# Performance work log

Measured on AMD Instinct MI355X. Metric: run time of the kernel, lower is better.

## Reference

```python
import jax, jax.numpy as jnp
import numpy as np
import math

EMBED = 1024
HEADS = 16
B, S = 2, 1024

def setup_inputs() -> dict:
    key = jax.random.key(0)
    ks = jax.random.split(key, 6)
    sc = 1.0 / math.sqrt(EMBED)
    return {
        "x": jax.random.normal(ks[0], (B, S, EMBED), dtype=jnp.float32),
        "Wq": jax.random.normal(ks[1], (EMBED, EMBED), dtype=jnp.float32) * sc,
        "Wk": jax.random.normal(ks[2], (EMBED, EMBED), dtype=jnp.float32) * sc,
        "Wv": jax.random.normal(ks[3], (EMBED, EMBED), dtype=jnp.float32) * sc,
        "Wo": jax.random.normal(ks[4], (EMBED, EMBED), dtype=jnp.float32) * sc,
        "bo": jax.random.normal(ks[5], (EMBED,), dtype=jnp.float32) * sc,
        "heads": HEADS,
    }

def reference(x, Wq, Wk, Wv, Wo, bo, heads):
    nB, nS, nE = x.shape
    nH = heads
    nG = nE // nH  # effective number of 'heads' in this (quirky) module

    def split(W):
        # (B,S,E) -> (B,S,G,H) -> (B,G,S,H); per-head dim is nH (as in source)
        return (x @ W).reshape(nB, nS, nG, nH).transpose(0, 2, 1, 3)

    q, k, v = split(Wq), split(Wk), split(Wv)
    # scale uses k.size(-1) == heads, matching the source
    att = jnp.einsum('bgsh,bgth->bgst', q, k) / math.sqrt(nH)
    causal = jnp.tril(jnp.ones((nS, nS), dtype=bool))  # True = keep
    att = jnp.where(causal, att, -jnp.inf)
    att = jax.nn.softmax(att, axis=-1)
    y = jnp.einsum('bgst,bgth->bgsh', att, v)
    y = y.transpose(0, 2, 1, 3).reshape(nB, nS, nE)
    return y @ Wo + bo
```

## Files before the change

### kernel.cpp

```cpp
#include <hip/hip_runtime.h>
#include <hip/hip_bf16.h>
#include <stdint.h>

typedef __attribute__((ext_vector_type(8))) short bf16x8;
typedef __attribute__((ext_vector_type(4))) short bf16x4;
typedef __attribute__((ext_vector_type(4))) float f32x4;

#define NB 2
#define SEQ 1024
#define EMB 1024
#define NH 16
#define NG 64

#if defined(__has_builtin)
#if __has_builtin(__builtin_amdgcn_mfma_f32_16x16x16bf16_1k)
#define QK_1K 1
#else
#define QK_1K 0
#endif
#if __has_builtin(__builtin_amdgcn_exp2f)
#define EXP2(x) __builtin_amdgcn_exp2f(x)
#else
#define EXP2(x) exp2f(x)
#endif
#if __has_builtin(__builtin_amdgcn_rcpf)
#define RCP(x) __builtin_amdgcn_rcpf(x)
#else
#define RCP(x) (1.0f / (x))
#endif
#else
#define QK_1K 0
#define EXP2(x) exp2f(x)
#define RCP(x) (1.0f / (x))
#endif

__device__ __forceinline__ unsigned short f2bf(float f){
  uint32_t u = __float_as_uint(f);
  uint32_t r = (u + 0x7fffu + ((u >> 16) & 1u)) >> 16;
  return (unsigned short)r;
}

__device__ __forceinline__ uint32_t pack_bf2(float lo, float hi){
  uint32_t a = (__float_as_uint(lo) + 0x8000u) >> 16;
  uint32_t b = (__float_as_uint(hi) + 0x8000u) & 0xffff0000u;
  return a | b;
}

__device__ __forceinline__ void gld_lds16(const void* g, void* l){
  __builtin_amdgcn_global_load_lds((__attribute__((address_space(1))) void*)(uintptr_t)(g),
                                   (__attribute__((address_space(3))) void*)(l),
                                   16, 0, 0);
}


__global__ __launch_bounds__(256) void prep_kernel(
    const float* __restrict__ x,
    const float* __restrict__ W0, const float* __restrict__ W1,
    const float* __restrict__ W2, const float* __restrict__ W3,
    unsigned short* __restrict__ xb,
    unsigned short* __restrict__ wtAll)
{
  const int bid = blockIdx.x;
  if (bid < 2048){
    int i = (bid * 256 + threadIdx.x) * 4;
    float4 f = *(const float4*)(x + i);
    ushort4 o;
    o.x = f2bf(f.x); o.y = f2bf(f.y); o.z = f2bf(f.z); o.w = f2bf(f.w);
    *(ushort4*)(xb + i) = o;
    return;
  }
  __shared__ float tile[32][33];
  const int b2 = bid - 2048;
  const int z = b2 & 3;
  const int rest = b2 >> 2;
  const float* W = (z == 0) ? W0 : (z == 1) ? W1 : (z == 2) ? W2 : W3;
  unsigned short* o = wtAll + (size_t)z * EMB * EMB;
  const int n0 = (rest & 31) * 32, k0 = (rest >> 5) * 32;
  const int tx = threadIdx.x & 31, ty = threadIdx.x >> 5;
#pragma unroll
  for (int i = 0; i < 4; i++)
    tile[ty + 8*i][tx] = W[(size_t)(k0 + ty + 8*i) * EMB + n0 + tx];
  __syncthreads();
#pragma unroll
  for (int i = 0; i < 4; i++)
    o[(size_t)(n0 + ty + 8*i) * EMB + k0 + tx] = f2bf(tile[tx][ty + 8*i]);
}


template<int J>
__device__ __forceinline__ void stage_tile(const unsigned short* __restrict__ src,
                                           unsigned short* __restrict__ dst,
                                           int row0, int k0, int t){
#pragma unroll
  for (int j = 0; j < J; ++j){
    const int c = t + 256 * j;
    const int row = c >> 3;
    const int col8 = (c & 7) ^ (row & 7);
    gld_lds16(src + (size_t)(row0 + row) * 1024 + k0 + col8 * 8, dst + c * 8);
  }
}


__global__ __launch_bounds__(256) void gemm_qkv_kernel(
    const unsigned short* __restrict__ A,
    const unsigned short* __restrict__ WtAll,
    unsigned short* __restrict__ qws,
    unsigned short* __restrict__ kws,
    unsigned short* __restrict__ vws)
{
  __shared__ unsigned short As[2][64][64];
  __shared__ unsigned short Bs[2][3][64][64];
  const unsigned short* B0 = WtAll;
  const unsigned short* B1 = WtAll + (size_t)EMB * EMB;
  const unsigned short* B2 = WtAll + (size_t)2 * EMB * EMB;
  const int m0 = blockIdx.x * 64, n0 = blockIdx.y * 64;
  const int t = threadIdx.x;
  const int l = t & 63, w = t >> 6;
  const int wr = w >> 1, wc = w & 1;
  const int lr = l & 15, lk = l >> 4;
  const int sw0 = (lk ^ (lr & 7)) * 8;
  const int sw1 = ((lk + 4) ^ (lr & 7)) * 8;

  f32x4 acc[3][2][2];
#pragma unroll
  for (int z = 0; z < 3; z++)
#pragma unroll
    for (int m = 0; m < 2; m++)
#pragma unroll
      for (int n = 0; n < 2; n++)
#pragma unroll
        for (int r = 0; r < 4; r++) acc[z][m][n][r] = 0.f;

  stage_tile<2>(A,  &As[0][0][0],    m0, 0, t);
  stage_tile<2>(B0, &Bs[0][0][0][0], n0, 0, t);
  stage_tile<2>(B1, &Bs[0][1][0][0], n0, 0, t);
  stage_tile<2>(B2, &Bs[0][2][0][0], n0, 0, t);
  __syncthreads();
  int cur = 0;
  for (int kt = 0; kt < 16; ++kt){
    if (kt < 15){
      const int k1 = (kt + 1) * 64;
      stage_tile<2>(A,  &As[cur^1][0][0],    m0, k1, t);
      stage_tile<2>(B0, &Bs[cur^1][0][0][0], n0, k1, t);
      stage_tile<2>(B1, &Bs[cur^1][1][0][0], n0, k1, t);
      stage_tile<2>(B2, &Bs[cur^1][2][0][0], n0, k1, t);
    }
#pragma unroll
    for (int half = 0; half < 2; ++half){
      const int sw = half ? sw1 : sw0;
      bf16x8 af[2];
#pragma unroll
      for (int m = 0; m < 2; m++)
        af[m] = *(const bf16x8*)(&As[cur][wr*32 + m*16 + lr][sw]);
#pragma unroll
      for (int z = 0; z < 3; z++){
        bf16x8 bfr[2];
#pragma unroll
        for (int n = 0; n < 2; n++)
          bfr[n] = *(const bf16x8*)(&Bs[cur][z][wc*32 + n*16 + lr][sw]);
#pragma unroll
        for (int m = 0; m < 2; m++)
#pragma unroll
          for (int n = 0; n < 2; n++)
            acc[z][m][n] = __builtin_amdgcn_mfma_f32_16x16x32_bf16(af[m], bfr[n], acc[z][m][n], 0, 0, 0);
      }
    }
    __syncthreads();
    cur ^= 1;
  }

  unsigned short (*vtile)[72] = (unsigned short (*)[72])(&As[0][0][0]);

#pragma unroll
  for (int m = 0; m < 2; m++){
    const int rowb = m0 + wr*32 + m*16 + lk*4;
#pragma unroll
    for (int n = 0; n < 2; n++){
      const int col = n0 + wc*32 + n*16 + lr;
      const int g = col >> 4, h = col & 15;
#pragma unroll
      for (int r = 0; r < 4; r++){
        const int rr = rowb + r;
        const int b = rr >> 10, s = rr & 1023;
        const int bg = b * NG + g;
        qws[((size_t)bg * 1024 + s) * 16 + h] = f2bf(acc[0][m][n][r] * 0.36067376022f);
        kws[((size_t)bg * 1024 + s) * 16 + h] = f2bf(acc[1][m][n][r]);
        vtile[wc*32 + n*16 + lr][wr*32 + m*16 + lk*4 + r] = f2bf(acc[2][m][n][r]);
      }
    }
  }
  __syncthreads();
  {
    const int cl = t >> 2, sc = t & 3;
    const int col = n0 + cl, g = col >> 4, h = col & 15;
    const int b = m0 >> 10;
    const int s0 = (m0 & 1023) + sc * 16;
    const int bg = b * NG + g;
    const uint4* p = (const uint4*)(&vtile[cl][sc * 16]);
    const uint4 v0 = p[0], v1 = p[1];
    uint4* dst = (uint4*)(vws + ((size_t)bg * 16 + h) * 1024 + s0);
    dst[0] = v0; dst[1] = v1;
  }
}


__global__ __launch_bounds__(256) void gemm_out_kernel(
    const unsigned short* __restrict__ A,
    const unsigned short* __restrict__ Bw,
    const float* __restrict__ bo,
    float* __restrict__ out)
{
  __shared__ unsigned short As[2][64][64];
  __shared__ unsigned short Bs[2][64][64];
  const int m0 = blockIdx.x * 64, n0 = blockIdx.y * 64;
  const int t = threadIdx.x;
  const int l = t & 63, w = t >> 6;
  const int wr = w >> 1, wc = w & 1;
  const int lr = l & 15, lk = l >> 4;
  const int sw0 = (lk ^ (lr & 7)) * 8;
  const int sw1 = ((lk + 4) ^ (lr & 7)) * 8;

  f32x4 acc[2][2];
#pragma unroll
  for (int m = 0; m < 2; m++)
#pragma unroll
    for (int n = 0; n < 2; n++)
#pragma unroll
      for (int r = 0; r < 4; r++) acc[m][n][r] = 0.f;

  stage_tile<2>(A, &As[0][0][0], m0, 0, t);
  stage_tile<2>(Bw, &Bs[0][0][0], n0, 0, t);
  __syncthreads();
  int cur = 0;
  for (int kt = 0; kt < 16; ++kt){
    if (kt < 15){
      stage_tile<2>(A, &As[cur ^ 1][0][0], m0, (kt + 1) * 64, t);
      stage_tile<2>(Bw, &Bs[cur ^ 1][0][0], n0, (kt + 1) * 64, t);
    }
#pragma unroll
    for (int half = 0; half < 2; ++half){
      const int sw = half ? sw1 : sw0;
      bf16x8 af[2], bfr[2];
#pragma unroll
      for (int m = 0; m < 2; m++) af[m]  = *(const bf16x8*)(&As[cur][wr*32 + m*16 + lr][sw]);
#pragma unroll
      for (int n = 0; n < 2; n++) bfr[n] = *(const bf16x8*)(&Bs[cur][wc*32 + n*16 + lr][sw]);
#pragma unroll
      for (int m = 0; m < 2; m++)
#pragma unroll
        for (int n = 0; n < 2; n++)
          acc[m][n] = __builtin_amdgcn_mfma_f32_16x16x32_bf16(af[m], bfr[n], acc[m][n], 0, 0, 0);
    }
    __syncthreads();
    cur ^= 1;
  }

#pragma unroll
  for (int m = 0; m < 2; m++){
    const int rowb = m0 + wr*32 + m*16 + lk*4;
#pragma unroll
    for (int n = 0; n < 2; n++){
      const int col = n0 + wc*32 + n*16 + lr;
      const float bb = bo[col];
#pragma unroll
      for (int r = 0; r < 4; r++)
        out[(size_t)(rowb + r) * 1024 + col] = acc[m][n][r] + bb;
    }
  }
}


#if QK_1K
struct KF { bf16x4 f[4]; };
#else
struct KF { bf16x8 f[4]; };
#endif

__device__ __forceinline__ void attn_tile(
#if QK_1K
    const bf16x4& aq,
#else
    const bf16x8& aq,
#endif
    const KF& kc, const bf16x8& bv0, const bf16x8& bv1,
    f32x4& yacc0, f32x4& yacc1, f32x4& sfr0, f32x4& sfr1,
    unsigned short (*pw)[72],
    int c0, int nt, int tt, int lr, int lk, const bf16x8& bone)
{
  const int t0 = tt << 6;
  f32x4 sacc[4];
#pragma unroll
  for (int ts = 0; ts < 4; ++ts){
    f32x4 zc;
#pragma unroll
    for (int r = 0; r < 4; r++) zc[r] = 0.f;
#if QK_1K
    sacc[ts] = __builtin_amdgcn_mfma_f32_16x16x16bf16_1k(kc.f[ts], aq, zc, 0, 0, 0);
#else
    sacc[ts] = __builtin_amdgcn_mfma_f32_16x16x32_bf16(kc.f[ts], aq, zc, 0, 0, 0);
#endif
  }

  if (tt == nt - 1){
    const int qrow = c0 + lr;
#pragma unroll
    for (int ts = 0; ts < 4; ++ts){
      const int key0 = t0 + ts*16 + lk*4;
#pragma unroll
      for (int r = 0; r < 4; ++r)
        if (key0 + r > qrow) sacc[ts][r] = -1e30f;
    }
  }

#pragma unroll
  for (int ts = 0; ts < 4; ++ts){
    const float e0 = EXP2(sacc[ts][0]);
    const float e1 = EXP2(sacc[ts][1]);
    const float e2 = EXP2(sacc[ts][2]);
    const float e3 = EXP2(sacc[ts][3]);
    uint2 u; u.x = pack_bf2(e0, e1); u.y = pack_bf2(e2, e3);
    *(uint2*)(&pw[lr][ts*16 + lk*4]) = u;
  }

  const bf16x8 ap0 = *(const bf16x8*)(&pw[lr][lk * 8]);
  const bf16x8 ap1 = *(const bf16x8*)(&pw[lr][32 + lk * 8]);

  sfr0  = __builtin_amdgcn_mfma_f32_16x16x32_bf16(ap0, bone,  sfr0, 0, 0, 0);
  sfr1  = __builtin_amdgcn_mfma_f32_16x16x32_bf16(ap1, bone,  sfr1, 0, 0, 0);
  yacc0 = __builtin_amdgcn_mfma_f32_16x16x32_bf16(ap0, bv0, yacc0, 0, 0, 0);
  yacc1 = __builtin_amdgcn_mfma_f32_16x16x32_bf16(ap1, bv1, yacc1, 0, 0, 0);
}

__global__ __launch_bounds__(256, 4) void attn_kernel(
    const unsigned short* __restrict__ q,
    const unsigned short* __restrict__ k,
    const unsigned short* __restrict__ vt,
    unsigned short* __restrict__ y)
{
  const int blk = blockIdx.x;
  const int bg = blk & 127;
  const int pg = blk >> 7;
  const int t = threadIdx.x, w = t >> 6, l = t & 63;
  const int lr = l & 15, lk = l >> 4;
  const int wvv = 31 - (pg * 4 + w);
  const int cA = 2 * wvv;
  const int c0A = cA * 16, c0B = c0A + 16;
  const int nt = (cA >> 2) + 1;

  __shared__ unsigned short p_lds[8][16][72];
  unsigned short (*pwA)[72] = p_lds[w * 2];
  unsigned short (*pwB)[72] = p_lds[w * 2 + 1];

  const unsigned short* qb = q + (size_t)bg * 1024 * 16;
  const unsigned short* kb = k + (size_t)bg * 1024 * 16;
  const unsigned short* vb = vt + (size_t)bg * 16 * 1024;
  const int b = bg >> 6, g = bg & 63;

  bf16x8 bone;
#pragma unroll
  for (int i = 0; i < 8; i++) bone[i] = (short)0x3F80;

#if QK_1K
  const bf16x4 aqA = *(const bf16x4*)(qb + (size_t)(c0A + lr) * 16 + lk * 4);
  const bf16x4 aqB = *(const bf16x4*)(qb + (size_t)(c0B + lr) * 16 + lk * 4);
#else
  bf16x8 aqA, aqB;
#pragma unroll
  for (int i = 0; i < 8; i++){ aqA[i] = 0; aqB[i] = 0; }
  if (lk < 2){
    aqA = *(const bf16x8*)(qb + (size_t)(c0A + lr) * 16 + lk * 8);
    aqB = *(const bf16x8*)(qb + (size_t)(c0B + lr) * 16 + lk * 8);
  }
#endif

  f32x4 yA0, yA1, sA0, sA1, yB0, yB1, sB0, sB1;
#pragma unroll
  for (int r = 0; r < 4; r++){
    yA0[r] = yA1[r] = sA0[r] = sA1[r] = 0.f;
    yB0[r] = yB1[r] = sB0[r] = sB1[r] = 0.f;
  }

  KF kc, kn;
#if !QK_1K
#pragma unroll
  for (int ts = 0; ts < 4; ++ts)
#pragma unroll
    for (int i = 0; i < 8; i++){ kc.f[ts][i] = 0; kn.f[ts][i] = 0; }
#endif
#pragma unroll
  for (int ts = 0; ts < 4; ++ts){
#if QK_1K
    kc.f[ts] = *(const bf16x4*)(kb + (size_t)(ts*16 + lr) * 16 + lk * 4);
#else
    if (lk < 2) kc.f[ts] = *(const bf16x8*)(kb + (size_t)(ts*16 + lr) * 16 + lk * 8);
#endif
  }

  for (int tt = 0; tt < nt; ++tt){
    const int t0 = tt << 6;

    if (tt + 1 < nt){
      const int t1 = t0 + 64;
#pragma unroll
      for (int ts = 0; ts < 4; ++ts){
#if QK_1K
        kn.f[ts] = *(const bf16x4*)(kb + (size_t)(t1 + ts*16 + lr) * 16 + lk * 4);
#else
        if (lk < 2) kn.f[ts] = *(const bf16x8*)(kb + (size_t)(t1 + ts*16 + lr) * 16 + lk * 8);
#endif
      }
    }
    const bf16x8 bv0 = *(const bf16x8*)(vb + (size_t)lr * 1024 + t0 + lk * 8);
    const bf16x8 bv1 = *(const bf16x8*)(vb + (size_t)lr * 1024 + t0 + 32 + lk * 8);

    attn_tile(aqA, kc, bv0, bv1, yA0, yA1, sA0, sA1, pwA, c0A, nt, tt, lr, lk, bone);
    attn_tile(aqB, kc, bv0, bv1, yB0, yB1, sB0, sB1, pwB, c0B, nt, tt, lr, lk, bone);

    kc = kn;
  }

#pragma unroll
  for (int r = 0; r < 4; ++r){
    const int sAi = c0A + lk*4 + r;
    const float vA = (yA0[r] + yA1[r]) * RCP(sA0[r] + sA1[r]);
    y[((size_t)b * 1024 + sAi) * 1024 + g * 16 + lr] = f2bf(vA);
    const int sBi = c0B + lk*4 + r;
    const float vB = (yB0[r] + yB1[r]) * RCP(sB0[r] + sB1[r]);
    y[((size_t)b * 1024 + sBi) * 1024 + g * 16 + lr] = f2bf(vB);
  }
}


extern "C" void kernel_launch(void* const* d_in, const int* in_sizes, int n_in,
                              void* d_out, int out_size, void* d_ws, size_t ws_size,
                              hipStream_t stream)
{
  const float* x  = (const float*)d_in[0];
  const float* Wq = (const float*)d_in[1];
  const float* Wk = (const float*)d_in[2];
  const float* Wv = (const float*)d_in[3];
  const float* Wo = (const float*)d_in[4];
  const float* bo = (const float*)d_in[5];
  float* out = (float*)d_out;
  char* ws = (char*)d_ws;

  unsigned short* xb  = (unsigned short*)(ws);
  unsigned short* wt  = (unsigned short*)(ws + (4u << 20));
  unsigned short* qws = (unsigned short*)(ws + (12u << 20));
  unsigned short* kws = (unsigned short*)(ws + (16u << 20));
  unsigned short* vws = (unsigned short*)(ws + (20u << 20));
  unsigned short* yws = (unsigned short*)(ws);

  prep_kernel<<<6144, 256, 0, stream>>>(x, Wq, Wk, Wv, Wo, xb, wt);
  gemm_qkv_kernel<<<dim3(32, 16), 256, 0, stream>>>(xb, wt, qws, kws, vws);
  attn_kernel<<<1024, 256, 0, stream>>>(qws, kws, vws, yws);
  gemm_out_kernel<<<dim3(32, 16), 256, 0, stream>>>(yws, wt + (size_t)3 * 1024 * 1024, bo, out);
}
```

Baseline: 67.41 us.

## Fuse all four stages into one cooperative persistent kernel with grid syncs

Replaces the four separate launches (convert/transpose, QKV GEMM, attention, output GEMM) with one cooperative kernel of 512 blocks that loops over virtual blocks and separates the stages with grid.sync(). This removes the launch gaps between kernels. To fit two blocks per CU in 32KB of shared memory, the QKV GEMM k-tile is halved to 32. The original multi-kernel path remains as a fallback if occupancy is too low or the cooperative launch fails. The tradeoff is grid-barrier cost plus fewer resident blocks, which may slow the attention and GEMM phases.

```diff
diff --git a/kernel.cpp b/kernel.cpp
--- a/kernel.cpp
+++ b/kernel.cpp
@@ -1,6 +1,9 @@
 #include <hip/hip_runtime.h>
 #include <hip/hip_bf16.h>
+#include <hip/hip_cooperative_groups.h>
 #include <stdint.h>
+
+namespace cg = cooperative_groups;
 
 typedef __attribute__((ext_vector_type(8))) short bf16x8;
 typedef __attribute__((ext_vector_type(4))) short bf16x4;
@@ -50,6 +53,393 @@
   __builtin_amdgcn_global_load_lds((__attribute__((address_space(1))) void*)(uintptr_t)(g),
                                    (__attribute__((address_space(3))) void*)(l),
                                    16, 0, 0);
+}
+
+
+template<int J>
+__device__ __forceinline__ void stage_tile(const unsigned short* __restrict__ src,
+                                           unsigned short* __restrict__ dst,
+                                           int row0, int k0, int t){
+#pragma unroll
+  for (int j = 0; j < J; ++j){
+    const int c = t + 256 * j;
+    const int row = c >> 3;
+    const int col8 = (c & 7) ^ (row & 7);
+    gld_lds16(src + (size_t)(row0 + row) * 1024 + k0 + col8 * 8, dst + c * 8);
+  }
+}
+
+__device__ __forceinline__ void stage_tile32(const unsigned short* __restrict__ src,
+                                             unsigned short* __restrict__ dst,
+                                             int row0, int k0, int t){
+  const int row = t >> 2;
+  const int col8 = (t & 3) ^ (row & 3);
+  gld_lds16(src + (size_t)(row0 + row) * 1024 + k0 + col8 * 8, dst + t * 8);
+}
+
+
+#if QK_1K
+struct KF { bf16x4 f[4]; };
+#else
+struct KF { bf16x8 f[4]; };
+#endif
+
+__device__ __forceinline__ void attn_tile(
+#if QK_1K
+    const bf16x4& aq,
+#else
+    const bf16x8& aq,
+#endif
+    const KF& kc, const bf16x8& bv0, const bf16x8& bv1,
+    f32x4& yacc0, f32x4& yacc1, f32x4& sfr0, f32x4& sfr1,
+    unsigned short (*pw)[72],
+    int c0, int nt, int tt, int lr, int lk, const bf16x8& bone)
+{
+  const int t0 = tt << 6;
+  f32x4 sacc[4];
+#pragma unroll
+  for (int ts = 0; ts < 4; ++ts){
+    f32x4 zc;
+#pragma unroll
+    for (int r = 0; r < 4; r++) zc[r] = 0.f;
+#if QK_1K
+    sacc[ts] = __builtin_amdgcn_mfma_f32_16x16x16bf16_1k(kc.f[ts], aq, zc, 0, 0, 0);
+#else
+    sacc[ts] = __builtin_amdgcn_mfma_f32_16x16x32_bf16(kc.f[ts], aq, zc, 0, 0, 0);
+#endif
+  }
+
+  if (tt == nt - 1){
+    const int qrow = c0 + lr;
+#pragma unroll
+    for (int ts = 0; ts < 4; ++ts){
+      const int key0 = t0 + ts*16 + lk*4;
+#pragma unroll
+      for (int r = 0; r < 4; ++r)
+        if (key0 + r > qrow) sacc[ts][r] = -1e30f;
+    }
+  }
+
+#pragma unroll
+  for (int ts = 0; ts < 4; ++ts){
+    const float e0 = EXP2(sacc[ts][0]);
+    const float e1 = EXP2(sacc[ts][1]);
+    const float e2 = EXP2(sacc[ts][2]);
+    const float e3 = EXP2(sacc[ts][3]);
+    uint2 u; u.x = pack_bf2(e0, e1); u.y = pack_bf2(e2, e3);
+    *(uint2*)(&pw[lr][ts*16 + lk*4]) = u;
+  }
+
+  const bf16x8 ap0 = *(const bf16x8*)(&pw[lr][lk * 8]);
+  const bf16x8 ap1 = *(const bf16x8*)(&pw[lr][32 + lk * 8]);
+
+  sfr0  = __builtin_amdgcn_mfma_f32_16x16x32_bf16(ap0, bone,  sfr0, 0, 0, 0);
+  sfr1  = __builtin_amdgcn_mfma_f32_16x16x32_bf16(ap1, bone,  sfr1, 0, 0, 0);
+  yacc0 = __builtin_amdgcn_mfma_f32_16x16x32_bf16(ap0, bv0, yacc0, 0, 0, 0);
+  yacc1 = __builtin_amdgcn_mfma_f32_16x16x32_bf16(ap1, bv1, yacc1, 0, 0, 0);
+}
+
+__device__ __forceinline__ void attn_pair(
+    const unsigned short* __restrict__ q,
+    const unsigned short* __restrict__ k,
+    const unsigned short* __restrict__ vt,
+    unsigned short* __restrict__ y,
+    int bg, int wvv, int lr, int lk,
+    unsigned short (*pwA)[72], unsigned short (*pwB)[72])
+{
+  const int cA = 2 * wvv;
+  const int c0A = cA * 16, c0B = c0A + 16;
+  const int nt = (cA >> 2) + 1;
+
+  const unsigned short* qb = q + (size_t)bg * 1024 * 16;
+  const unsigned short* kb = k + (size_t)bg * 1024 * 16;
+  const unsigned short* vb = vt + (size_t)bg * 16 * 1024;
+  const int b = bg >> 6, g = bg & 63;
+
+  bf16x8 bone;
+#pragma unroll
+  for (int i = 0; i < 8; i++) bone[i] = (short)0x3F80;
+
+#if QK_1K
+  const bf16x4 aqA = *(const bf16x4*)(qb + (size_t)(c0A + lr) * 16 + lk * 4);
+  const bf16x4 aqB = *(const bf16x4*)(qb + (size_t)(c0B + lr) * 16 + lk * 4);
+#else
+  bf16x8 aqA, aqB;
+#pragma unroll
+  for (int i = 0; i < 8; i++){ aqA[i] = 0; aqB[i] = 0; }
+  if (lk < 2){
+    aqA = *(const bf16x8*)(qb + (size_t)(c0A + lr) * 16 + lk * 8);
+    aqB = *(const bf16x8*)(qb + (size_t)(c0B + lr) * 16 + lk * 8);
+  }
+#endif
+
+  f32x4 yA0, yA1, sA0, sA1, yB0, yB1, sB0, sB1;
+#pragma unroll
+  for (int r = 0; r < 4; r++){
+    yA0[r] = yA1[r] = sA0[r] = sA1[r] = 0.f;
+    yB0[r] = yB1[r] = sB0[r] = sB1[r] = 0.f;
+  }
+
+  KF kc, kn;
+#if !QK_1K
+#pragma unroll
+  for (int ts = 0; ts < 4; ++ts)
+#pragma unroll
+    for (int i = 0; i < 8; i++){ kc.f[ts][i] = 0; kn.f[ts][i] = 0; }
+#endif
+#pragma unroll
+  for (int ts = 0; ts < 4; ++ts){
+#if QK_1K
+    kc.f[ts] = *(const bf16x4*)(kb + (size_t)(ts*16 + lr) * 16 + lk * 4);
+#else
+    if (lk < 2) kc.f[ts] = *(const bf16x8*)(kb + (size_t)(ts*16 + lr) * 16 + lk * 8);
+#endif
+  }
+
+  for (int tt = 0; tt < nt; ++tt){
+    const int t0 = tt << 6;
+    if (tt + 1 < nt){
+      const int t1 = t0 + 64;
+#pragma unroll
+      for (int ts = 0; ts < 4; ++ts){
+#if QK_1K
+        kn.f[ts] = *(const bf16x4*)(kb + (size_t)(t1 + ts*16 + lr) * 16 + lk * 4);
+#else
+        if (lk < 2) kn.f[ts] = *(const bf16x8*)(kb + (size_t)(t1 + ts*16 + lr) * 16 + lk * 8);
+#endif
+      }
+    }
+    const bf16x8 bv0 = *(const bf16x8*)(vb + (size_t)lr * 1024 + t0 + lk * 8);
+    const bf16x8 bv1 = *(const bf16x8*)(vb + (size_t)lr * 1024 + t0 + 32 + lk * 8);
+
+    attn_tile(aqA, kc, bv0, bv1, yA0, yA1, sA0, sA1, pwA, c0A, nt, tt, lr, lk, bone);
+    attn_tile(aqB, kc, bv0, bv1, yB0, yB1, sB0, sB1, pwB, c0B, nt, tt, lr, lk, bone);
+
+    kc = kn;
+  }
+
+#pragma unroll
+  for (int r = 0; r < 4; ++r){
+    const int sAi = c0A + lk*4 + r;
+    const float vA = (yA0[r] + yA1[r]) * RCP(sA0[r] + sA1[r]);
+    y[((size_t)b * 1024 + sAi) * 1024 + g * 16 + lr] = f2bf(vA);
+    const int sBi = c0B + lk*4 + r;
+    const float vB = (yB0[r] + yB1[r]) * RCP(sB0[r] + sB1[r]);
+    y[((size_t)b * 1024 + sBi) * 1024 + g * 16 + lr] = f2bf(vB);
+  }
+}
+
+
+__global__ __launch_bounds__(256, 2) void mega_kernel(
+    const float* __restrict__ x,
+    const float* __restrict__ W0, const float* __restrict__ W1,
+    const float* __restrict__ W2, const float* __restrict__ W3,
+    const float* __restrict__ bo, float* __restrict__ out,
+    unsigned short* __restrict__ xb,
+    unsigned short* __restrict__ wt,
+    unsigned short* __restrict__ qws,
+    unsigned short* __restrict__ kws,
+    unsigned short* __restrict__ vws)
+{
+  cg::grid_group grid = cg::this_grid();
+  __shared__ __align__(16) unsigned char smem[32768];
+
+  const int blk = blockIdx.x;
+  const int t = threadIdx.x;
+  const int l = t & 63, w = t >> 6;
+  const int lr = l & 15, lk = l >> 4;
+
+  for (int vb = blk; vb < 6144; vb += 512){
+    if (vb < 2048){
+      const int i = (vb * 256 + t) * 4;
+      float4 f = *(const float4*)(x + i);
+      ushort4 o;
+      o.x = f2bf(f.x); o.y = f2bf(f.y); o.z = f2bf(f.z); o.w = f2bf(f.w);
+      *(ushort4*)(xb + i) = o;
+    } else {
+      float (*tile)[33] = (float (*)[33])smem;
+      const int b2 = vb - 2048;
+      const int z = b2 & 3;
+      const int rest = b2 >> 2;
+      const float* W = (z == 0) ? W0 : (z == 1) ? W1 : (z == 2) ? W2 : W3;
+      unsigned short* o = wt + (size_t)z * EMB * EMB;
+      const int n0 = (rest & 31) * 32, k0 = (rest >> 5) * 32;
+      const int tx = t & 31, ty = t >> 5;
+      __syncthreads();
+#pragma unroll
+      for (int i = 0; i < 4; i++)
+        tile[ty + 8*i][tx] = W[(size_t)(k0 + ty + 8*i) * EMB + n0 + tx];
+      __syncthreads();
+#pragma unroll
+      for (int i = 0; i < 4; i++)
+        o[(size_t)(n0 + ty + 8*i) * EMB + k0 + tx] = f2bf(tile[tx][ty + 8*i]);
+    }
+  }
+  grid.sync();
+
+  {
+    unsigned short (*As)[64][32] = (unsigned short (*)[64][32])smem;
+    unsigned short (*Bs)[3][64][32] = (unsigned short (*)[3][64][32])(smem + 8192);
+    const unsigned short* A = xb;
+    const unsigned short* B0 = wt;
+    const unsigned short* B1 = wt + (size_t)EMB * EMB;
+    const unsigned short* B2 = wt + (size_t)2 * EMB * EMB;
+    const int m0 = (blk >> 4) * 64, n0 = (blk & 15) * 64;
+    const int wr = w >> 1, wc = w & 1;
+    const int sw = (lk ^ (lr & 3)) * 8;
+
+    f32x4 acc[3][2][2];
+#pragma unroll
+    for (int z = 0; z < 3; z++)
+#pragma unroll
+      for (int m = 0; m < 2; m++)
+#pragma unroll
+        for (int n = 0; n < 2; n++)
+#pragma unroll
+          for (int r = 0; r < 4; r++) acc[z][m][n][r] = 0.f;
+
+    stage_tile32(A,  &As[0][0][0],    m0, 0, t);
+    stage_tile32(B0, &Bs[0][0][0][0], n0, 0, t);
+    stage_tile32(B1, &Bs[0][1][0][0], n0, 0, t);
+    stage_tile32(B2, &Bs[0][2][0][0], n0, 0, t);
+    __syncthreads();
+    int cur = 0;
+    for (int kt = 0; kt < 32; ++kt){
+      if (kt < 31){
+        const int k1 = (kt + 1) * 32;
+        stage_tile32(A,  &As[cur^1][0][0],    m0, k1, t);
+        stage_tile32(B0, &Bs[cur^1][0][0][0], n0, k1, t);
+        stage_tile32(B1, &Bs[cur^1][1][0][0], n0, k1, t);
+        stage_tile32(B2, &Bs[cur^1][2][0][0], n0, k1, t);
+      }
+      bf16x8 af[2];
+#pragma unroll
+      for (int m = 0; m < 2; m++)
+        af[m] = *(const bf16x8*)(&As[cur][wr*32 + m*16 + lr][sw]);
+#pragma unroll
+      for (int z = 0; z < 3; z++){
+        bf16x8 bfr[2];
+#pragma unroll
+        for (int n = 0; n < 2; n++)
+          bfr[n] = *(const bf16x8*)(&Bs[cur][z][wc*32 + n*16 + lr][sw]);
+#pragma unroll
+        for (int m = 0; m < 2; m++)
+#pragma unroll
+          for (int n = 0; n < 2; n++)
+            acc[z][m][n] = __builtin_amdgcn_mfma_f32_16x16x32_bf16(af[m], bfr[n], acc[z][m][n], 0, 0, 0);
+      }
+      __syncthreads();
+      cur ^= 1;
+    }
+
+    unsigned short (*vtile)[72] = (unsigned short (*)[72])smem;
+#pragma unroll
+    for (int m = 0; m < 2; m++){
+      const int rowb = m0 + wr*32 + m*16 + lk*4;
+#pragma unroll
+      for (int n = 0; n < 2; n++){
+        const int col = n0 + wc*32 + n*16 + lr;
+        const int g = col >> 4, h = col & 15;
+#pragma unroll
+        for (int r = 0; r < 4; r++){
+          const int rr = rowb + r;
+          const int b = rr >> 10, s = rr & 1023;
+          const int bg = b * NG + g;
+          qws[((size_t)bg * 1024 + s) * 16 + h] = f2bf(acc[0][m][n][r] * 0.36067376022f);
+          kws[((size_t)bg * 1024 + s) * 16 + h] = f2bf(acc[1][m][n][r]);
+          vtile[wc*32 + n*16 + lr][wr*32 + m*16 + lk*4 + r] = f2bf(acc[2][m][n][r]);
+        }
+      }
+    }
+    __syncthreads();
+    {
+      const int cl = t >> 2, sc = t & 3;
+      const int col = n0 + cl, g = col >> 4, h = col & 15;
+      const int b = m0 >> 10;
+      const int s0 = (m0 & 1023) + sc * 16;
+      const int bg = b * NG + g;
+      const uint4* p = (const uint4*)(&vtile[cl][sc * 16]);
+      const uint4 v0 = p[0], v1 = p[1];
+      uint4* dst = (uint4*)(vws + ((size_t)bg * 16 + h) * 1024 + s0);
+      dst[0] = v0; dst[1] = v1;
+    }
+  }
+  grid.sync();
+
+  {
+    unsigned short (*pl)[16][72] = (unsigned short (*)[16][72])smem;
+    unsigned short (*pwA)[72] = pl[w * 2];
+    unsigned short (*pwB)[72] = pl[w * 2 + 1];
+    const int bg = blk & 127;
+    const int g0 = blk >> 7;
+#pragma unroll
+    for (int it = 0; it < 2; ++it){
+      const int pgeff = it ? (7 - g0) : g0;
+      const int wvv = 31 - (pgeff * 4 + w);
+      attn_pair(qws, kws, vws, xb , bg, wvv, lr, lk, pwA, pwB);
+    }
+  }
+  grid.sync();
+
+  {
+    unsigned short (*As)[64][64] = (unsigned short (*)[64][64])smem;
+    unsigned short (*Bs)[64][64] = (unsigned short (*)[64][64])(smem + 16384);
+    const unsigned short* A = xb;
+    const unsigned short* Bw = wt + (size_t)3 * EMB * EMB;
+    const int m0 = (blk >> 4) * 64, n0 = (blk & 15) * 64;
+    const int wr = w >> 1, wc = w & 1;
+    const int sw0 = (lk ^ (lr & 7)) * 8;
+    const int sw1 = ((lk + 4) ^ (lr & 7)) * 8;
+
+    f32x4 acc[2][2];
+#pragma unroll
+    for (int m = 0; m < 2; m++)
+#pragma unroll
+      for (int n = 0; n < 2; n++)
+#pragma unroll
+        for (int r = 0; r < 4; r++) acc[m][n][r] = 0.f;
+
+    __syncthreads();
+    stage_tile<2>(A,  &As[0][0][0], m0, 0, t);
+    stage_tile<2>(Bw, &Bs[0][0][0], n0, 0, t);
+    __syncthreads();
+    int cur = 0;
+    for (int kt = 0; kt < 16; ++kt){
+      if (kt < 15){
+        stage_tile<2>(A,  &As[cur ^ 1][0][0], m0, (kt + 1) * 64, t);
+        stage_tile<2>(Bw, &Bs[cur ^ 1][0][0], n0, (kt + 1) * 64, t);
+      }
+#pragma unroll
+      for (int half = 0; half < 2; ++half){
+        const int sw = half ? sw1 : sw0;
+        bf16x8 af[2], bfr[2];
+#pragma unroll
+        for (int m = 0; m < 2; m++) af[m]  = *(const bf16x8*)(&As[cur][wr*32 + m*16 + lr][sw]);
+#pragma unroll
+        for (int n = 0; n < 2; n++) bfr[n] = *(const bf16x8*)(&Bs[cur][wc*32 + n*16 + lr][sw]);
+#pragma unroll
+        for (int m = 0; m < 2; m++)
+#pragma unroll
+          for (int n = 0; n < 2; n++)
+            acc[m][n] = __builtin_amdgcn_mfma_f32_16x16x32_bf16(af[m], bfr[n], acc[m][n], 0, 0, 0);
+      }
+      __syncthreads();
+      cur ^= 1;
+    }
+
+#pragma unroll
+    for (int m = 0; m < 2; m++){
+      const int rowb = m0 + wr*32 + m*16 + lk*4;
+#pragma unroll
+      for (int n = 0; n < 2; n++){
+        const int col = n0 + wc*32 + n*16 + lr;
+        const float bb = bo[col];
+#pragma unroll
+        for (int r = 0; r < 4; r++)
+          out[(size_t)(rowb + r) * 1024 + col] = acc[m][n][r] + bb;
+      }
+    }
+  }
 }
 
 
@@ -85,21 +475,6 @@
   for (int i = 0; i < 4; i++)
     o[(size_t)(n0 + ty + 8*i) * EMB + k0 + tx] = f2bf(tile[tx][ty + 8*i]);
 }
-
-
-template<int J>
-__device__ __forceinline__ void stage_tile(const unsigned short* __restrict__ src,
-                                           unsigned short* __restrict__ dst,
-                                           int row0, int k0, int t){
-#pragma unroll
-  for (int j = 0; j < J; ++j){
-    const int c = t + 256 * j;
-    const int row = c >> 3;
-    const int col8 = (c & 7) ^ (row & 7);
-    gld_lds16(src + (size_t)(row0 + row) * 1024 + k0 + col8 * 8, dst + c * 8);
-  }
-}
-
 
 __global__ __launch_bounds__(256) void gemm_qkv_kernel(
     const unsigned short* __restrict__ A,
@@ -170,7 +545,6 @@
   }
 
   unsigned short (*vtile)[72] = (unsigned short (*)[72])(&As[0][0][0]);
-
 #pragma unroll
   for (int m = 0; m < 2; m++){
     const int rowb = m0 + wr*32 + m*16 + lk*4;
@@ -202,7 +576,6 @@
     dst[0] = v0; dst[1] = v1;
   }
 }
-
 
 __global__ __launch_bounds__(256) void gemm_out_kernel(
     const unsigned short* __restrict__ A,
@@ -269,68 +642,6 @@
   }
 }
 
-
-#if QK_1K
-struct KF { bf16x4 f[4]; };
-#else
-struct KF { bf16x8 f[4]; };
-#endif
-
-__device__ __forceinline__ void attn_tile(
-#if QK_1K
-    const bf16x4& aq,
-#else
-    const bf16x8& aq,
-#endif
-    const KF& kc, const bf16x8& bv0, const bf16x8& bv1,
-    f32x4& yacc0, f32x4& yacc1, f32x4& sfr0, f32x4& sfr1,
-    unsigned short (*pw)[72],
-    int c0, int nt, int tt, int lr, int lk, const bf16x8& bone)
-{
-  const int t0 = tt << 6;
-  f32x4 sacc[4];
-#pragma unroll
-  for (int ts = 0; ts < 4; ++ts){
-    f32x4 zc;
-#pragma unroll
-    for (int r = 0; r < 4; r++) zc[r] = 0.f;
-#if QK_1K
-    sacc[ts] = __builtin_amdgcn_mfma_f32_16x16x16bf16_1k(kc.f[ts], aq, zc, 0, 0, 0);
-#else
-    sacc[ts] = __builtin_amdgcn_mfma_f32_16x16x32_bf16(kc.f[ts], aq, zc, 0, 0, 0);
-#endif
-  }
-
-  if (tt == nt - 1){
-    const int qrow = c0 + lr;
-#pragma unroll
-    for (int ts = 0; ts < 4; ++ts){
-      const int key0 = t0 + ts*16 + lk*4;
-#pragma unroll
-      for (int r = 0; r < 4; ++r)
-        if (key0 + r > qrow) sacc[ts][r] = -1e30f;
-    }
-  }
-
-#pragma unroll
-  for (int ts = 0; ts < 4; ++ts){
-    const float e0 = EXP2(sacc[ts][0]);
-    const float e1 = EXP2(sacc[ts][1]);
-    const float e2 = EXP2(sacc[ts][2]);
-    const float e3 = EXP2(sacc[ts][3]);
-    uint2 u; u.x = pack_bf2(e0, e1); u.y = pack_bf2(e2, e3);
-    *(uint2*)(&pw[lr][ts*16 + lk*4]) = u;
-  }
-
-  const bf16x8 ap0 = *(const bf16x8*)(&pw[lr][lk * 8]);
-  const bf16x8 ap1 = *(const bf16x8*)(&pw[lr][32 + lk * 8]);
-
-  sfr0  = __builtin_amdgcn_mfma_f32_16x16x32_bf16(ap0, bone,  sfr0, 0, 0, 0);
-  sfr1  = __builtin_amdgcn_mfma_f32_16x16x32_bf16(ap1, bone,  sfr1, 0, 0, 0);
-  yacc0 = __builtin_amdgcn_mfma_f32_16x16x32_bf16(ap0, bv0, yacc0, 0, 0, 0);
-  yacc1 = __builtin_amdgcn_mfma_f32_16x16x32_bf16(ap1, bv1, yacc1, 0, 0, 0);
-}
-
 __global__ __launch_bounds__(256, 4) void attn_kernel(
     const unsigned short* __restrict__ q,
     const unsigned short* __restrict__ k,
@@ -343,91 +654,12 @@
   const int t = threadIdx.x, w = t >> 6, l = t & 63;
   const int lr = l & 15, lk = l >> 4;
   const int wvv = 31 - (pg * 4 + w);
-  const int cA = 2 * wvv;
-  const int c0A = cA * 16, c0B = c0A + 16;
-  const int nt = (cA >> 2) + 1;
 
   __shared__ unsigned short p_lds[8][16][72];
   unsigned short (*pwA)[72] = p_lds[w * 2];
   unsigned short (*pwB)[72] = p_lds[w * 2 + 1];
 
-  const unsigned short* qb = q + (size_t)bg * 1024 * 16;
-  const unsigned short* kb = k + (size_t)bg * 1024 * 16;
-  const unsigned short* vb = vt + (size_t)bg * 16 * 1024;
-  const int b = bg >> 6, g = bg & 63;
-
-  bf16x8 bone;
-#pragma unroll
-  for (int i = 0; i < 8; i++) bone[i] = (short)0x3F80;
-
-#if QK_1K
-  const bf16x4 aqA = *(const bf16x4*)(qb + (size_t)(c0A + lr) * 16 + lk * 4);
-  const bf16x4 aqB = *(const bf16x4*)(qb + (size_t)(c0B + lr) * 16 + lk * 4);
-#else
-  bf16x8 aqA, aqB;
-#pragma unroll
-  for (int i = 0; i < 8; i++){ aqA[i] = 0; aqB[i] = 0; }
-  if (lk < 2){
-    aqA = *(const bf16x8*)(qb + (size_t)(c0A + lr) * 16 + lk * 8);
-    aqB = *(const bf16x8*)(qb + (size_t)(c0B + lr) * 16 + lk * 8);
-  }
-#endif
-
-  f32x4 yA0, yA1, sA0, sA1, yB0, yB1, sB0, sB1;
-#pragma unroll
-  for (int r = 0; r < 4; r++){
-    yA0[r] = yA1[r] = sA0[r] = sA1[r] = 0.f;
-    yB0[r] = yB1[r] = sB0[r] = sB1[r] = 0.f;
-  }
-
-  KF kc, kn;
-#if !QK_1K
-#pragma unroll
-  for (int ts = 0; ts < 4; ++ts)
-#pragma unroll
-    for (int i = 0; i < 8; i++){ kc.f[ts][i] = 0; kn.f[ts][i] = 0; }
-#endif
-#pragma unroll
-  for (int ts = 0; ts < 4; ++ts){
-#if QK_1K
-    kc.f[ts] = *(const bf16x4*)(kb + (size_t)(ts*16 + lr) * 16 + lk * 4);
-#else
-    if (lk < 2) kc.f[ts] = *(const bf16x8*)(kb + (size_t)(ts*16 + lr) * 16 + lk * 8);
-#endif
-  }
-
-  for (int tt = 0; tt < nt; ++tt){
-    const int t0 = tt << 6;
-
-    if (tt + 1 < nt){
-      const int t1 = t0 + 64;
-#pragma unroll
-      for (int ts = 0; ts < 4; ++ts){
-#if QK_1K
-        kn.f[ts] = *(const bf16x4*)(kb + (size_t)(t1 + ts*16 + lr) * 16 + lk * 4);
-#else
-        if (lk < 2) kn.f[ts] = *(const bf16x8*)(kb + (size_t)(t1 + ts*16 + lr) * 16 + lk * 8);
-#endif
-      }
-    }
-    const bf16x8 bv0 = *(const bf16x8*)(vb + (size_t)lr * 1024 + t0 + lk * 8);
-    const bf16x8 bv1 = *(const bf16x8*)(vb + (size_t)lr * 1024 + t0 + 32 + lk * 8);
-
-    attn_tile(aqA, kc, bv0, bv1, yA0, yA1, sA0, sA1, pwA, c0A, nt, tt, lr, lk, bone);
-    attn_tile(aqB, kc, bv0, bv1, yB0, yB1, sB0, sB1, pwB, c0B, nt, tt, lr, lk, bone);
-
-    kc = kn;
-  }
-
-#pragma unroll
-  for (int r = 0; r < 4; ++r){
-    const int sAi = c0A + lk*4 + r;
-    const float vA = (yA0[r] + yA1[r]) * RCP(sA0[r] + sA1[r]);
-    y[((size_t)b * 1024 + sAi) * 1024 + g * 16 + lr] = f2bf(vA);
-    const int sBi = c0B + lk*4 + r;
-    const float vB = (yB0[r] + yB1[r]) * RCP(sB0[r] + sB1[r]);
-    y[((size_t)b * 1024 + sBi) * 1024 + g * 16 + lr] = f2bf(vB);
-  }
+  attn_pair(q, k, vt, y, bg, wvv, lr, lk, pwA, pwB);
 }
 
 
@@ -449,10 +681,25 @@
   unsigned short* qws = (unsigned short*)(ws + (12u << 20));
   unsigned short* kws = (unsigned short*)(ws + (16u << 20));
   unsigned short* vws = (unsigned short*)(ws + (20u << 20));
-  unsigned short* yws = (unsigned short*)(ws);
+
+  int nb = 0;
+  hipError_t qerr = hipOccupancyMaxActiveBlocksPerMultiprocessor(
+      &nb, (const void*)mega_kernel, 256, 0);
+  bool coop_ok = (qerr == hipSuccess) && (nb >= 2);
+
+  if (coop_ok){
+    void* args[] = {
+      (void*)&x, (void*)&Wq, (void*)&Wk, (void*)&Wv, (void*)&Wo,
+      (void*)&bo, (void*)&out,
+      (void*)&xb, (void*)&wt, (void*)&qws, (void*)&kws, (void*)&vws
+    };
+    hipError_t lerr = hipLaunchCooperativeKernel((void*)mega_kernel, dim3(512), dim3(256),
+                                                 args, 0, stream);
+    if (lerr == hipSuccess) return;
+  }
 
   prep_kernel<<<6144, 256, 0, stream>>>(x, Wq, Wk, Wv, Wo, xb, wt);
   gemm_qkv_kernel<<<dim3(32, 16), 256, 0, stream>>>(xb, wt, qws, kws, vws);
-  attn_kernel<<<1024, 256, 0, stream>>>(qws, kws, vws, yws);
-  gemm_out_kernel<<<dim3(32, 16), 256, 0, stream>>>(yws, wt + (size_t)3 * 1024 * 1024, bo, out);
-}
+  attn_kernel<<<1024, 256, 0, stream>>>(qws, kws, vws, xb);
+  gemm_out_kernel<<<dim3(32, 16), 256, 0, stream>>>(xb, wt + (size_t)3 * EMB * EMB, bo, out);
+}
```

After: 247.3 us. 3.67x slower.
